# Kernel tuning notes

Measured on AMD Instinct MI355X. Metric: run time of the kernel, lower is better.

## Reference

```python
import jax, jax.numpy as jnp
import numpy as np

N_NODES = 100000
N_EDGES = 1600000
IN_FEATS = 128
HEADS = 4
OUT_FEATS = 32
NEG_SLOPE = 0.2


def setup_inputs() -> dict:
    key = jax.random.key(0)
    ks = jax.random.split(key, 7)
    x = jax.random.normal(ks[0], (N_NODES, IN_FEATS), dtype=jnp.float32)
    fc_w = jax.random.normal(ks[1], (HEADS * OUT_FEATS, IN_FEATS), dtype=jnp.float32) * (1.0 / np.sqrt(IN_FEATS))
    attn_l = jax.random.normal(ks[2], (HEADS, OUT_FEATS), dtype=jnp.float32) * (1.0 / np.sqrt(OUT_FEATS))
    attn_r = jax.random.normal(ks[3], (HEADS, OUT_FEATS), dtype=jnp.float32) * (1.0 / np.sqrt(OUT_FEATS))
    bias = jnp.zeros((HEADS * OUT_FEATS,), dtype=jnp.float32)
    src = jax.random.randint(ks[4], (N_EDGES,), 0, N_NODES, dtype=jnp.int64 if jax.config.jax_enable_x64 else jnp.int32)
    dst = jax.random.randint(ks[5], (N_EDGES,), 0, N_NODES, dtype=jnp.int64 if jax.config.jax_enable_x64 else jnp.int32)
    return {"x": x, "fc_w": fc_w, "attn_l": attn_l, "attn_r": attn_r, "bias": bias, "src": src, "dst": dst}


def reference(x, fc_w, attn_l, attn_r, bias, src, dst):
    """DGL GATConv (feat_drop=attn_drop=0, residual identity since in==H*D,
    allow_zero_in_degree=True, activation=None), then concat heads."""
    N = x.shape[0]
    H, D = attn_l.shape
    # linear projection: [N, H, D]
    feat = (x @ fc_w.T).reshape(N, H, D)
    # per-node attention halves: [N, H]
    el = jnp.einsum('nhd,hd->nh', feat, attn_l)
    er = jnp.einsum('nhd,hd->nh', feat, attn_r)
    # per-edge score with leaky relu: [E, H]
    e = el[src] + er[dst]
    e = jnp.where(e > 0, e, NEG_SLOPE * e)
    # edge softmax grouped by destination node
    emax = jax.ops.segment_max(e, dst, num_segments=N)          # [N, H]
    ee = jnp.exp(e - emax[dst])                                  # [E, H]
    denom = jax.ops.segment_sum(ee, dst, num_segments=N)        # [N, H]
    a = ee / jnp.maximum(denom[dst], jnp.float32(1e-38))         # [E, H]
    # weighted message + scatter aggregate: [N, H, D]
    msg = feat[src] * a[:, :, None]
    rst = jax.ops.segment_sum(msg, dst, num_segments=N)
    # residual (identity since in_feats == H*D) + bias
    rst = rst + x.reshape(N, H, D) + bias.reshape(1, H, D)
    # concat heads
    return rst.reshape(N, H * D)
```

## Files before the change

kernel.cpp:

```cpp
#include <hip/hip_runtime.h>
#include <math.h>

#define NEG_SLOPE 0.2f
#define PB 256
#define BKT_SHIFT 8

typedef __attribute__((ext_vector_type(8))) short bf16x8;
typedef __attribute__((ext_vector_type(4))) float f32x4;

__device__ __forceinline__ unsigned bf16_rne(float f) {
  unsigned u = __float_as_uint(f);
  return (u + 0x7fff + ((u >> 16) & 1)) >> 16;
}

__device__ __forceinline__ float lrelu_exp(float v) {
  v = v > 0.f ? v : NEG_SLOPE * v;
  return __expf(v);
}

__global__ __launch_bounds__(256) void gemm_feat_attn(
    const float* __restrict__ x, const unsigned* __restrict__ fc_wb,
    const float* __restrict__ attn_l, const float* __restrict__ attn_r,
    unsigned* __restrict__ featb, float* __restrict__ el,
    float* __restrict__ er, int N)
{
  __shared__ __align__(16) unsigned w_lds[128 * 68];
  const int t = threadIdx.x;
  const int row_base = blockIdx.x * 64;

  {
    const uint4* fb4 = reinterpret_cast<const uint4*>(fc_wb);
#pragma unroll
    for (int k = 0; k < 8; ++k) {
      const int i4 = t + k * 256;
      const uint4 v = fb4[i4];
      const int row = i4 >> 4;
      unsigned* d = &w_lds[row * 68 + (i4 & 15) * 4];
      d[0] = v.x; d[1] = v.y; d[2] = v.z; d[3] = v.w;
    }
  }

  const int w = t >> 6;
  const int l = t & 63;
  const int cl = l & 15;
  const int g = l >> 4;

  const int arow = min(row_base + w * 16 + cl, N - 1);
  const float* __restrict__ xp = x + (size_t)arow * 128;
  bf16x8 a_frag[4];
#pragma unroll
  for (int ks = 0; ks < 4; ++ks) {
    const float4 v0 = *reinterpret_cast<const float4*>(xp + ks * 32 + g * 8);
    const float4 v1 =
        *reinterpret_cast<const float4*>(xp + ks * 32 + g * 8 + 4);
    uint4 uu;
    uu.x = bf16_rne(v0.x) | (bf16_rne(v0.y) << 16);
    uu.y = bf16_rne(v0.z) | (bf16_rne(v0.w) << 16);
    uu.z = bf16_rne(v1.x) | (bf16_rne(v1.y) << 16);
    uu.w = bf16_rne(v1.z) | (bf16_rne(v1.w) << 16);
    a_frag[ks] = *reinterpret_cast<bf16x8*>(&uu);
  }
  __syncthreads();

  f32x4 acc[8];
#pragma unroll
  for (int ct = 0; ct < 8; ++ct) acc[ct] = (f32x4){0.f, 0.f, 0.f, 0.f};

#pragma unroll
  for (int ct = 0; ct < 8; ++ct) {
#pragma unroll
    for (int ks = 0; ks < 4; ++ks) {
      const bf16x8 b_frag = *reinterpret_cast<const bf16x8*>(
          &w_lds[(ct * 16 + cl) * 68 + ks * 16 + g * 4]);
      acc[ct] = __builtin_amdgcn_mfma_f32_16x16x32_bf16(a_frag[ks], b_frag,
                                                        acc[ct], 0, 0, 0);
    }
  }

#pragma unroll
  for (int ct = 0; ct < 8; ++ct) {
#pragma unroll
    for (int r = 0; r < 4; ++r) {
      const float v = acc[ct][r];
      const float vn = __shfl_xor(v, 1);
      const int node = row_base + w * 16 + g * 4 + r;
      if ((cl & 1) == 0 && node < N) {
        featb[(size_t)node * 64 + ct * 8 + (cl >> 1)] =
            bf16_rne(v) | (bf16_rne(vn) << 16);
      }
    }
  }

  float al_lo[4], al_hi[4], ar_lo[4], ar_hi[4];
#pragma unroll
  for (int h = 0; h < 4; ++h) {
    al_lo[h] = attn_l[h * 32 + cl];
    al_hi[h] = attn_l[h * 32 + 16 + cl];
    ar_lo[h] = attn_r[h * 32 + cl];
    ar_hi[h] = attn_r[h * 32 + 16 + cl];
  }
#pragma unroll
  for (int r = 0; r < 4; ++r) {
    const int node = row_base + w * 16 + g * 4 + r;
#pragma unroll
    for (int h = 0; h < 4; ++h) {
      float pl = acc[2 * h][r] * al_lo[h] + acc[2 * h + 1][r] * al_hi[h];
      float pr = acc[2 * h][r] * ar_lo[h] + acc[2 * h + 1][r] * ar_hi[h];
#pragma unroll
      for (int d = 1; d < 16; d <<= 1) {
        pl += __shfl_xor(pl, d);
        pr += __shfl_xor(pr, d);
      }
      if (cl == 0 && node < N) {
        el[(size_t)node * 4 + h] = pl;
        er[(size_t)node * 4 + h] = pr;
      }
    }
  }
}

__global__ __launch_bounds__(256) void hist_bucket(const int* __restrict__ dst,
                                                   int* __restrict__ hist,
                                                   const float* __restrict__ fc_w,
                                                   unsigned* __restrict__ fc_wb,
                                                   int E, int NB, int chunk) {
  __shared__ int h[512];
  const int k = blockIdx.x, t = threadIdx.x;
  if (k < 32) {
    const int i = k * 256 + t;
    const float2 v = reinterpret_cast<const float2*>(fc_w)[i];
    fc_wb[i] = bf16_rne(v.x) | (bf16_rne(v.y) << 16);
  }
  for (int i = t; i < NB; i += 256) h[i] = 0;
  __syncthreads();
  const int beg = k * chunk, end = min(E, beg + chunk);
  for (int e = beg + t; e < end; e += 256)
    atomicAdd(&h[dst[e] >> BKT_SHIFT], 1);
  __syncthreads();
  for (int i = t; i < NB; i += 256) hist[i * PB + k] = h[i];
}

__global__ __launch_bounds__(256) void scan_a(const int* __restrict__ deg,
                                              int* __restrict__ offs,
                                              int* __restrict__ blk_sums,
                                              int n) {
  __shared__ int wsum[4];
  const int b = blockIdx.x, t = threadIdx.x;
  const int base = b * 2048 + t * 8;
  int v[8];
  int s = 0;
#pragma unroll
  for (int j = 0; j < 8; ++j) {
    v[j] = s;
    const int d = (base + j < n) ? deg[base + j] : 0;
    s += d;
  }
  const int lane = t & 63;
  int incl = s;
#pragma unroll
  for (int d = 1; d < 64; d <<= 1) {
    const int o = __shfl_up(incl, d);
    if (lane >= d) incl += o;
  }
  const int w = t >> 6;
  if (lane == 63) wsum[w] = incl;
  __syncthreads();
  int woff = 0;
  for (int ww = 0; ww < w; ++ww) woff += wsum[ww];
  const int thr_excl = woff + incl - s;
#pragma unroll
  for (int j = 0; j < 8; ++j)
    if (base + j < n) offs[base + j] = thr_excl + v[j];
  if (t == 255) blk_sums[b] = woff + incl;
}

__global__ void scan_b(const int* __restrict__ blk_sums,
                       int* __restrict__ blk_off, int* __restrict__ offs,
                       int n, int nb) {
  const int lane = threadIdx.x & 63;
  int v = (lane < nb) ? blk_sums[lane] : 0;
  int incl = v;
#pragma unroll
  for (int d = 1; d < 64; d <<= 1) {
    const int o = __shfl_up(incl, d);
    if (lane >= d) incl += o;
  }
  if (lane < nb) blk_off[lane] = incl - v;
  if (lane == 63) offs[n] = incl;
}

__global__ __launch_bounds__(256) void part_scatter(
    const int* __restrict__ src, const int* __restrict__ dst,
    const int* __restrict__ hscan, const int* __restrict__ blk_off,
    unsigned* __restrict__ part, int E, int NB, int chunk) {
  __shared__ int cur[512];
  const int k = blockIdx.x, t = threadIdx.x;
  for (int i = t; i < NB; i += 256) {
    const int m = i * PB + k;
    cur[i] = hscan[m] + blk_off[m >> 11];
  }
  __syncthreads();
  const int beg = k * chunk, end = min(E, beg + chunk);
  for (int e = beg + t; e < end; e += 256) {
    const int d = dst[e];
    const int b = d >> BKT_SHIFT;
    const int pos = atomicAdd(&cur[b], 1);
    part[pos] = (unsigned)src[e] |
                ((unsigned)(d & ((1 << BKT_SHIFT) - 1)) << 20);
  }
}

__global__ __launch_bounds__(512) void build_csr(
    const unsigned* __restrict__ part, const int* __restrict__ hscan,
    const int* __restrict__ blk_off, const float* __restrict__ el,
    const float* __restrict__ er, int* __restrict__ node_offs,
    unsigned* __restrict__ csr, uint2* __restrict__ wsb,
    int N, int E, int NB) {
  __shared__ int cnt[256];
  __shared__ int wtot[4];
  const int b = blockIdx.x, t = threadIdx.x;
  const int m0 = b * PB;
  const int bbase = hscan[m0] + blk_off[m0 >> 11];
  int bend = E;
  if (b + 1 < NB) {
    const int m1 = (b + 1) * PB;
    bend = hscan[m1] + blk_off[m1 >> 11];
  }
  const int node0 = b << BKT_SHIFT;
  if (t < 256) cnt[t] = 0;
  __syncthreads();
  for (int p = bbase + t; p < bend; p += 512)
    atomicAdd(&cnt[part[p] >> 20], 1);
  __syncthreads();
  int a0 = 0, incl = 0;
  if (t < 256) {
    a0 = cnt[t];
    incl = a0;
#pragma unroll
    for (int d1 = 1; d1 < 64; d1 <<= 1) {
      const int o = __shfl_up(incl, d1);
      if ((t & 63) >= d1) incl += o;
    }
    if ((t & 63) == 63) wtot[t >> 6] = incl;
  }
  __syncthreads();
  if (t < 256) {
    const int w = t >> 6;
    int woff = 0;
    for (int ww = 0; ww < w; ++ww) woff += wtot[ww];
    const int e0 = woff + incl - a0;
    cnt[t] = e0;
    if (node0 + t < N) node_offs[node0 + t] = bbase + e0;
    if (b == NB - 1 && t == 0) node_offs[N] = E;
  }
  __syncthreads();
  for (int p = bbase + t; p < bend; p += 512) {
    const unsigned v = part[p];
    const unsigned ld = v >> 20;
    const unsigned s = v & 0xFFFFFu;
    const int lpos = atomicAdd(&cnt[ld], 1);
    const int pos = bbase + lpos;
    csr[pos] = v;
    const float4 l4 = *reinterpret_cast<const float4*>(el + s * 4);
    const float4 r4 =
        *reinterpret_cast<const float4*>(er + (unsigned)(node0 + ld) * 4);
    uint2 u;
    u.x = bf16_rne(lrelu_exp(l4.x + r4.x)) |
          (bf16_rne(lrelu_exp(l4.y + r4.y)) << 16);
    u.y = bf16_rne(lrelu_exp(l4.z + r4.z)) |
          (bf16_rne(lrelu_exp(l4.w + r4.w)) << 16);
    wsb[pos] = u;
  }
}

__global__ __launch_bounds__(256) void agg_kernel(
    const uint2* __restrict__ featb2, const unsigned* __restrict__ csr,
    const unsigned short* __restrict__ wsb_us, const float* __restrict__ x,
    const float* __restrict__ bias, const int* __restrict__ node_offs,
    float* __restrict__ out, int N, int E)
{
  const int n = (int)((blockIdx.x * (size_t)blockDim.x + threadIdx.x) >> 6);
  if (n >= N) return;
  const unsigned lane = threadIdx.x & 63;
  const unsigned half = lane >> 5;
  const unsigned li = lane & 31;
  const unsigned hh = li >> 3;
  const unsigned short* __restrict__ wp = wsb_us + hh;
  const int beg = node_offs[n];
  const int end = node_offs[n + 1];
  const int nfull = (end - beg) >> 3;

  float a0 = 0.f, a1 = 0.f, a2 = 0.f, a3 = 0.f, ds = 0.f;
  int p = beg;
  for (int gi = 0; gi < nfull; ++gi, p += 8) {
    unsigned pk[4]; unsigned wu[4]; uint2 fv[4];
#pragma unroll
    for (int i = 0; i < 4; ++i) pk[i] = csr[(unsigned)p + 2 * i + half];
#pragma unroll
    for (int i = 0; i < 4; ++i)
      wu[i] = wp[((unsigned)p + 2 * i + half) * 4];
#pragma unroll
    for (int i = 0; i < 4; ++i)
      fv[i] = featb2[(pk[i] & 0xFFFFFu) * 32 + li];
#pragma unroll
    for (int i = 0; i < 4; ++i) {
      const float w = __uint_as_float(wu[i] << 16);
      a0 = fmaf(w, __uint_as_float(fv[i].x << 16), a0);
      a1 = fmaf(w, __uint_as_float(fv[i].x & 0xffff0000u), a1);
      a2 = fmaf(w, __uint_as_float(fv[i].y << 16), a2);
      a3 = fmaf(w, __uint_as_float(fv[i].y & 0xffff0000u), a3);
      ds += w;
    }
  }
  if (p < end) {
    const int last = end - 1;
#pragma unroll
    for (int i = 0; i < 4; ++i) {
      const int e = p + 2 * i + (int)half;
      const unsigned ec = (unsigned)min(e, last);
      const unsigned pk = csr[ec];
      float w = __uint_as_float((unsigned)wp[ec * 4] << 16);
      if (e > last) w = 0.f;
      const uint2 fv = featb2[(pk & 0xFFFFFu) * 32 + li];
      a0 = fmaf(w, __uint_as_float(fv.x << 16), a0);
      a1 = fmaf(w, __uint_as_float(fv.x & 0xffff0000u), a1);
      a2 = fmaf(w, __uint_as_float(fv.y << 16), a2);
      a3 = fmaf(w, __uint_as_float(fv.y & 0xffff0000u), a3);
      ds += w;
    }
  }

  a0 += __shfl_xor(a0, 32);
  a1 += __shfl_xor(a1, 32);
  a2 += __shfl_xor(a2, 32);
  a3 += __shfl_xor(a3, 32);
  ds += __shfl_xor(ds, 32);

  if (half == 0) {
    const float inv = 1.f / fmaxf(ds, 1e-38f);
    const float4 xr = ((const float4*)x)[(unsigned)n * 32 + li];
    const float4 br = ((const float4*)bias)[li];
    float4 o;
    o.x = fmaf(a0, inv, xr.x + br.x);
    o.y = fmaf(a1, inv, xr.y + br.y);
    o.z = fmaf(a2, inv, xr.z + br.z);
    o.w = fmaf(a3, inv, xr.w + br.w);
    ((float4*)out)[(unsigned)n * 32 + li] = o;
  }
}

extern "C" void kernel_launch(void* const* d_in, const int* in_sizes, int n_in,
                              void* d_out, int out_size, void* d_ws,
                              size_t ws_size, hipStream_t stream) {
  const float* x      = (const float*)d_in[0];
  const float* fc_w   = (const float*)d_in[1];
  const float* attn_l = (const float*)d_in[2];
  const float* attn_r = (const float*)d_in[3];
  const float* bias   = (const float*)d_in[4];
  const int*   src    = (const int*)d_in[5];
  const int*   dst    = (const int*)d_in[6];
  const int N = in_sizes[0] / 128;
  const int E = in_sizes[5];
  float* out = (float*)d_out;

  const int NB = (N + 255) >> 8;
  const int M = NB * PB;
  const int chunk = (E + PB - 1) / PB;

  char* ws = (char*)d_ws;
  size_t off = 0;
  auto alloc = [&](size_t bytes) {
    void* p = ws + off;
    off += (bytes + 255) & ~(size_t)255;
    return p;
  };
  unsigned* featb   = (unsigned*)alloc((size_t)N * 128 * 2);
  unsigned* fc_wb   = (unsigned*)alloc(128 * 64 * 4);
  float* el         = (float*)alloc((size_t)N * 4 * 4);
  float* er         = (float*)alloc((size_t)N * 4 * 4);
  int*   hist       = (int*)alloc((size_t)M * 4);
  int*   hscan      = (int*)alloc((size_t)(M + 1) * 4);
  int*   node_offs  = (int*)alloc((size_t)(N + 1) * 4);
  int*   blk_sums   = (int*)alloc(256);
  int*   blk_off    = (int*)alloc(256);
  unsigned* part    = (unsigned*)alloc((size_t)E * 4);
  unsigned* csr     = (unsigned*)alloc((size_t)E * 4);
  uint2* wsb        = (uint2*)alloc((size_t)E * 8);

  hist_bucket<<<PB, 256, 0, stream>>>(dst, hist, fc_w, fc_wb, E, NB, chunk);
  gemm_feat_attn<<<(N + 63) / 64, 256, 0, stream>>>(x, fc_wb, attn_l, attn_r,
                                                    featb, el, er, N);
  const int nb = (M + 2047) / 2048;
  scan_a<<<nb, 256, 0, stream>>>(hist, hscan, blk_sums, M);
  scan_b<<<1, 64, 0, stream>>>(blk_sums, blk_off, hscan, M, nb);
  part_scatter<<<PB, 256, 0, stream>>>(src, dst, hscan, blk_off, part, E, NB,
                                       chunk);
  build_csr<<<NB, 512, 0, stream>>>(part, hscan, blk_off, el, er, node_offs,
                                    csr, wsb, N, E, NB);
  agg_kernel<<<(N + 3) / 4, 256, 0, stream>>>((const uint2*)featb, csr,
                                              (const unsigned short*)wsb, x,
                                              bias, node_offs, out, N, E);
}
```

Before: 168.4 us.

## Fold block-offset scan into consumers and split edge weight computation into sliced kernel

Removes the single-wavefront scan_b kernel by having each consumer kernel redo the tiny block-offset scan into shared memory. It also splits build_csr into a pure CSR permutation kernel and a separate compute_w kernel that computes the edge attention exponentials over 8 slices per bucket. The slicing gives much more parallelism for the gather-heavy el/er loads, since build_csr only launches about 391 blocks. In exchange the csr array is read back from memory, one more launch is added, and the offset scan is repeated in every block.

```diff
diff --git a/kernel.cpp b/kernel.cpp
--- a/kernel.cpp
+++ b/kernel.cpp
@@ -4,6 +4,7 @@
 #define NEG_SLOPE 0.2f
 #define PB 256
 #define BKT_SHIFT 8
+#define WSLICES 8
 
 typedef __attribute__((ext_vector_type(8))) short bf16x8;
 typedef __attribute__((ext_vector_type(4))) float f32x4;
@@ -16,6 +17,20 @@
 __device__ __forceinline__ float lrelu_exp(float v) {
   v = v > 0.f ? v : NEG_SLOPE * v;
   return __expf(v);
+}
+
+__device__ __forceinline__ void local_blk_scan(const int* __restrict__ blk_sums,
+                                               int* s_blk_off, int nb, int t) {
+  if (t < 64) {
+    const int v = (t < nb) ? blk_sums[t] : 0;
+    int incl = v;
+#pragma unroll
+    for (int d = 1; d < 64; d <<= 1) {
+      const int o = __shfl_up(incl, d);
+      if (t >= d) incl += o;
+    }
+    s_blk_off[t] = incl - v;
+  }
 }
 
 __global__ __launch_bounds__(256) void gemm_feat_attn(
@@ -174,30 +189,18 @@
   if (t == 255) blk_sums[b] = woff + incl;
 }
 
-__global__ void scan_b(const int* __restrict__ blk_sums,
-                       int* __restrict__ blk_off, int* __restrict__ offs,
-                       int n, int nb) {
-  const int lane = threadIdx.x & 63;
-  int v = (lane < nb) ? blk_sums[lane] : 0;
-  int incl = v;
-#pragma unroll
-  for (int d = 1; d < 64; d <<= 1) {
-    const int o = __shfl_up(incl, d);
-    if (lane >= d) incl += o;
-  }
-  if (lane < nb) blk_off[lane] = incl - v;
-  if (lane == 63) offs[n] = incl;
-}
-
 __global__ __launch_bounds__(256) void part_scatter(
     const int* __restrict__ src, const int* __restrict__ dst,
-    const int* __restrict__ hscan, const int* __restrict__ blk_off,
-    unsigned* __restrict__ part, int E, int NB, int chunk) {
+    const int* __restrict__ hscan, const int* __restrict__ blk_sums,
+    unsigned* __restrict__ part, int E, int NB, int chunk, int nb) {
   __shared__ int cur[512];
+  __shared__ int s_blk_off[64];
   const int k = blockIdx.x, t = threadIdx.x;
+  local_blk_scan(blk_sums, s_blk_off, nb, t);
+  __syncthreads();
   for (int i = t; i < NB; i += 256) {
     const int m = i * PB + k;
-    cur[i] = hscan[m] + blk_off[m >> 11];
+    cur[i] = hscan[m] + s_blk_off[m >> 11];
   }
   __syncthreads();
   const int beg = k * chunk, end = min(E, beg + chunk);
@@ -210,57 +213,78 @@
   }
 }
 
-__global__ __launch_bounds__(512) void build_csr(
+__global__ __launch_bounds__(256) void build_csr(
     const unsigned* __restrict__ part, const int* __restrict__ hscan,
-    const int* __restrict__ blk_off, const float* __restrict__ el,
-    const float* __restrict__ er, int* __restrict__ node_offs,
-    unsigned* __restrict__ csr, uint2* __restrict__ wsb,
-    int N, int E, int NB) {
+    const int* __restrict__ blk_sums, int* __restrict__ node_offs,
+    unsigned* __restrict__ csr, int N, int E, int NB, int nb) {
   __shared__ int cnt[256];
   __shared__ int wtot[4];
+  __shared__ int s_blk_off[64];
   const int b = blockIdx.x, t = threadIdx.x;
+  local_blk_scan(blk_sums, s_blk_off, nb, t);
+  if (t < 256) cnt[t] = 0;
+  __syncthreads();
   const int m0 = b * PB;
-  const int bbase = hscan[m0] + blk_off[m0 >> 11];
+  const int bbase = hscan[m0] + s_blk_off[m0 >> 11];
   int bend = E;
   if (b + 1 < NB) {
     const int m1 = (b + 1) * PB;
-    bend = hscan[m1] + blk_off[m1 >> 11];
+    bend = hscan[m1] + s_blk_off[m1 >> 11];
   }
   const int node0 = b << BKT_SHIFT;
-  if (t < 256) cnt[t] = 0;
-  __syncthreads();
-  for (int p = bbase + t; p < bend; p += 512)
+  for (int p = bbase + t; p < bend; p += 256)
     atomicAdd(&cnt[part[p] >> 20], 1);
   __syncthreads();
-  int a0 = 0, incl = 0;
-  if (t < 256) {
-    a0 = cnt[t];
-    incl = a0;
-#pragma unroll
-    for (int d1 = 1; d1 < 64; d1 <<= 1) {
-      const int o = __shfl_up(incl, d1);
-      if ((t & 63) >= d1) incl += o;
-    }
-    if ((t & 63) == 63) wtot[t >> 6] = incl;
-  }
-  __syncthreads();
-  if (t < 256) {
-    const int w = t >> 6;
-    int woff = 0;
-    for (int ww = 0; ww < w; ++ww) woff += wtot[ww];
-    const int e0 = woff + incl - a0;
-    cnt[t] = e0;
-    if (node0 + t < N) node_offs[node0 + t] = bbase + e0;
-    if (b == NB - 1 && t == 0) node_offs[N] = E;
-  }
-  __syncthreads();
-  for (int p = bbase + t; p < bend; p += 512) {
+  const int a0 = cnt[t];
+  int incl = a0;
+#pragma unroll
+  for (int d1 = 1; d1 < 64; d1 <<= 1) {
+    const int o = __shfl_up(incl, d1);
+    if ((t & 63) >= d1) incl += o;
+  }
+  const int w = t >> 6;
+  if ((t & 63) == 63) wtot[w] = incl;
+  __syncthreads();
+  int woff = 0;
+  for (int ww = 0; ww < w; ++ww) woff += wtot[ww];
+  const int e0 = woff + incl - a0;
+  cnt[t] = e0;
+  if (node0 + t < N) node_offs[node0 + t] = bbase + e0;
+  if (b == NB - 1 && t == 0) node_offs[N] = E;
+  __syncthreads();
+  for (int p = bbase + t; p < bend; p += 256) {
     const unsigned v = part[p];
+    const int lpos = atomicAdd(&cnt[v >> 20], 1);
+    csr[bbase + lpos] = v;
+  }
+}
+
+__global__ __launch_bounds__(256) void compute_w(
+    const unsigned* __restrict__ csr, const int* __restrict__ hscan,
+    const int* __restrict__ blk_sums, const float* __restrict__ el,
+    const float* __restrict__ er, uint2* __restrict__ wsb, int E, int NB,
+    int nb) {
+  __shared__ int s_blk_off[64];
+  const int b = blockIdx.x / WSLICES;
+  const int sl = blockIdx.x - b * WSLICES;
+  local_blk_scan(blk_sums, s_blk_off, nb, (int)threadIdx.x);
+  __syncthreads();
+  const int m0 = b * PB;
+  const int bbase = hscan[m0] + s_blk_off[m0 >> 11];
+  int bend = E;
+  if (b + 1 < NB) {
+    const int m1 = (b + 1) * PB;
+    bend = hscan[m1] + s_blk_off[m1 >> 11];
+  }
+  const int node0 = b << BKT_SHIFT;
+  const int len = bend - bbase;
+  const int per = (len + WSLICES - 1) / WSLICES;
+  const int s0 = bbase + sl * per;
+  const int s1 = min(bend, s0 + per);
+  for (int pos = s0 + (int)threadIdx.x; pos < s1; pos += 256) {
+    const unsigned v = csr[pos];
+    const unsigned s = v & 0xFFFFFu;
     const unsigned ld = v >> 20;
-    const unsigned s = v & 0xFFFFFu;
-    const int lpos = atomicAdd(&cnt[ld], 1);
-    const int pos = bbase + lpos;
-    csr[pos] = v;
     const float4 l4 = *reinterpret_cast<const float4*>(el + s * 4);
     const float4 r4 =
         *reinterpret_cast<const float4*>(er + (unsigned)(node0 + ld) * 4);
@@ -366,6 +390,7 @@
   const int NB = (N + 255) >> 8;
   const int M = NB * PB;
   const int chunk = (E + PB - 1) / PB;
+  const int nb = (M + 2047) / 2048;
 
   char* ws = (char*)d_ws;
   size_t off = 0;
@@ -382,7 +407,6 @@
   int*   hscan      = (int*)alloc((size_t)(M + 1) * 4);
   int*   node_offs  = (int*)alloc((size_t)(N + 1) * 4);
   int*   blk_sums   = (int*)alloc(256);
-  int*   blk_off    = (int*)alloc(256);
   unsigned* part    = (unsigned*)alloc((size_t)E * 4);
   unsigned* csr     = (unsigned*)alloc((size_t)E * 4);
   uint2* wsb        = (uint2*)alloc((size_t)E * 8);
@@ -390,13 +414,13 @@
   hist_bucket<<<PB, 256, 0, stream>>>(dst, hist, fc_w, fc_wb, E, NB, chunk);
   gemm_feat_attn<<<(N + 63) / 64, 256, 0, stream>>>(x, fc_wb, attn_l, attn_r,
                                                     featb, el, er, N);
-  const int nb = (M + 2047) / 2048;
   scan_a<<<nb, 256, 0, stream>>>(hist, hscan, blk_sums, M);
-  scan_b<<<1, 64, 0, stream>>>(blk_sums, blk_off, hscan, M, nb);
-  part_scatter<<<PB, 256, 0, stream>>>(src, dst, hscan, blk_off, part, E, NB,
-                                       chunk);
-  build_csr<<<NB, 512, 0, stream>>>(part, hscan, blk_off, el, er, node_offs,
-                                    csr, wsb, N, E, NB);
+  part_scatter<<<PB, 256, 0, stream>>>(src, dst, hscan, blk_sums, part, E,
+                                       NB, chunk, nb);
+  build_csr<<<NB, 256, 0, stream>>>(part, hscan, blk_sums, node_offs, csr, N,
+                                    E, NB, nb);
+  compute_w<<<NB * WSLICES, 256, 0, stream>>>(csr, hscan, blk_sums, el, er,
+                                              wsb, E, NB, nb);
   agg_kernel<<<(N + 3) / 4, 256, 0, stream>>>((const uint2*)featb, csr,
                                               (const unsigned short*)wsb, x,
                                               bias, node_offs, out, N, E);
```

New measurement: 159.7 us. 5.2% less time.
